# Performance work log

Hardware: AMD Instinct MI355X
Metric: run time of the kernel (lower is better)

The kernel has to match this reference:

```python
import jax, jax.numpy as jnp
import numpy as np

B, S, D, H = 2, 2048, 1024, 16


def setup_inputs() -> dict:
    key = jax.random.key(0)
    kq, kk, kv1, kv2 = jax.random.split(key, 4)
    return {
        "q": jax.random.normal(kq, (B, S, D), dtype=jnp.float32),
        "k": jax.random.normal(kk, (B, S, D), dtype=jnp.float32),
        "v1": jax.random.normal(kv1, (B, S, D), dtype=jnp.float32),
        "v2": jax.random.normal(kv2, (B, S, D), dtype=jnp.float32),
        "num_attn_heads": 16,
    }


def _split_heads(x, h):
    b, s, d = x.shape
    return x.reshape(b, s, h, d // h).transpose(0, 2, 1, 3)  # [B,H,S,dh]


def reference(q, k, v1, v2, num_attn_heads):
    h = num_attn_heads
    b, s, d = q.shape
    dh = d // h
    qh = _split_heads(q, h)
    kh = _split_heads(k, h)
    v1h = _split_heads(v1, h)
    v2h = _split_heads(v2, h)
    scores = jnp.einsum("bhqd,bhkd->bhqk", qh, kh) / jnp.sqrt(jnp.float32(dh))
    # Faithful to create_mask(input, 0): nopeek = triu(ones, k=0); mask = (nopeek == 0)
    # -> only STRICTLY lower triangle is visible; diagonal and above get -1e9.
    # Row 0 is fully masked -> softmax uniform (same as torch behavior).
    allowed = jnp.tril(jnp.ones((s, s), dtype=bool), k=-1)  # [S,S] j < i
    scores = jnp.where(allowed[None, None], scores, jnp.float32(-1e9))
    p_attn = jax.nn.softmax(scores, axis=-1)  # dropout p=0.0 -> identity
    o1 = jnp.einsum("bhqk,bhkd->bhqd", p_attn, v1h)
    o2 = jnp.einsum("bhqk,bhkd->bhqd", p_attn, v2h)
    o1 = o1.transpose(0, 2, 1, 3).reshape(b, s, d)
    o2 = o2.transpose(0, 2, 1, 3).reshape(b, s, d)
    return (o1, o2)
```

## Files before the change

kernel.cpp:

```cpp
#include <hip/hip_runtime.h>

#define B_ 2
#define S_ 2048
#define D_ 1024
#define H_ 16
#define DH 64
#define OFF2 (B_ * S_ * D_)
#define ELEMS (B_ * H_ * S_ * DH)

typedef __attribute__((ext_vector_type(8))) __bf16 bf16x8;
typedef __attribute__((ext_vector_type(4))) float f32x4;
typedef __attribute__((ext_vector_type(4))) unsigned int u32x4;
typedef __attribute__((ext_vector_type(2))) unsigned int u32x2;
typedef __attribute__((address_space(3))) unsigned int lds_u32;
typedef __attribute__((address_space(1))) const unsigned int glob_u32;

__device__ __forceinline__ unsigned short f2bf(float f) {
    return __builtin_bit_cast(unsigned short, (__bf16)f);
}
__device__ __forceinline__ unsigned int pk2(float a, float b) {
    return (unsigned int)f2bf(a) | ((unsigned int)f2bf(b) << 16);
}
__device__ __forceinline__ float bf2f(unsigned short h) {
    unsigned int u = ((unsigned int)h) << 16;
    return __builtin_bit_cast(float, u);
}

__global__ void prep_all(const float* __restrict__ q, const float* __restrict__ k,
                         const float* __restrict__ v1, const float* __restrict__ v2,
                         unsigned short* __restrict__ qb, unsigned short* __restrict__ kb,
                         unsigned short* __restrict__ v1t, unsigned short* __restrict__ v2t) {
    int id = blockIdx.x;
    if (id < 4096) {
        int ysel = id & 1;
        int cid = (id >> 1) * 256 + threadIdx.x;
        const float* src = ysel ? k : q;
        unsigned short* dst = ysel ? kb : qb;
        float scale = ysel ? 1.0f : 0.125f * 1.4426950408889634f;
        int d8 = cid & 7;
        int s  = (cid >> 3) & (S_ - 1);
        int h  = (cid >> 14) & (H_ - 1);
        int b  = cid >> 18;
        int off = (b * S_ + s) * D_ + h * DH + d8 * 8;
        float4 f0 = *(const float4*)(src + off);
        float4 f1 = *(const float4*)(src + off + 4);
        u32x4 wv = {pk2(f0.x * scale, f0.y * scale), pk2(f0.z * scale, f0.w * scale),
                    pk2(f1.x * scale, f1.y * scale), pk2(f1.z * scale, f1.w * scale)};
        *(u32x4*)(dst + cid * 8) = wv;
        return;
    }
    __shared__ __align__(16) unsigned short ldsT[64][72];
    int id2 = id - 4096;
    int t = threadIdx.x;
    int s0 = (id2 & 31) * 64;
    int bh = (id2 >> 5) & 31;
    int b = bh >> 4, h = bh & 15;
    const float* src = (id2 >> 10) ? v2 : v1;
    unsigned short* dst = (id2 >> 10) ? v2t : v1t;
    {
        int sl = t >> 2, dc = t & 3;
        int off = (b * S_ + s0 + sl) * D_ + h * DH + dc * 16;
#pragma unroll
        for (int i4 = 0; i4 < 4; i4++) {
            float4 f = *(const float4*)(src + off + i4 * 4);
            int d = dc * 16 + i4 * 4;
            ldsT[d + 0][sl] = f2bf(f.x);
            ldsT[d + 1][sl] = f2bf(f.y);
            ldsT[d + 2][sl] = f2bf(f.z);
            ldsT[d + 3][sl] = f2bf(f.w);
        }
    }
    __syncthreads();
    {
        int d = t >> 2, sc = t & 3;
        u32x4 a = *(const u32x4*)(&ldsT[d][sc * 16]);
        u32x4 c = *(const u32x4*)(&ldsT[d][sc * 16 + 8]);
        int off = (bh * DH + d) * S_ + s0 + sc * 16;
        *(u32x4*)(dst + off) = a;
        *(u32x4*)(dst + off + 8) = c;
    }
}

__global__ __launch_bounds__(256) void flash_attn(
        const unsigned short* __restrict__ qb, const unsigned short* __restrict__ kb,
        const unsigned short* __restrict__ v1t, const unsigned short* __restrict__ v2t,
        float* __restrict__ out) {
    __shared__ __align__(16) unsigned short sK0[4096], sK1[4096];
    __shared__ __align__(16) unsigned short sV1[4096], sV2[4096];

    int tid = threadIdx.x;
    int w = tid >> 6, lane = tid & 63;
    int lr = lane & 15, lg = lane >> 4;
    int srow = tid >> 3, sco = tid & 7;

    int id = blockIdx.x;
    int xcd = id & 7;
    int j = id >> 3;
    int bh = xcd * 4 + (j & 3);
    int qt = 31 - (j >> 2);
    int b = bh >> 4, hh = bh & 15;

    const unsigned short* gK  = kb  + bh * (S_ * DH);
    const unsigned short* gV1 = v1t + bh * (DH * S_);
    const unsigned short* gV2 = v2t + bh * (DH * S_);

    auto stageV = [&](int t) {
#pragma unroll
        for (int jj = 0; jj < 2; jj++) {
            int row = srow + jj * 32;
            int cosw = (sco ^ (row & 7)) * 8;
            int c8 = (tid + jj * 256) * 8;
            __builtin_amdgcn_global_load_lds((glob_u32*)(gV1 + row * S_ + t * 64 + cosw),
                                             (lds_u32*)(sV1 + c8), 16, 0, 0);
            __builtin_amdgcn_global_load_lds((glob_u32*)(gV2 + row * S_ + t * 64 + cosw),
                                             (lds_u32*)(sV2 + c8), 16, 0, 0);
        }
    };
    auto stageK = [&](unsigned short* dK, int t) {
#pragma unroll
        for (int jj = 0; jj < 2; jj++) {
            int row = srow + jj * 32;
            int cosw = (sco ^ (row & 7)) * 8;
            int c8 = (tid + jj * 256) * 8;
            __builtin_amdgcn_global_load_lds((glob_u32*)(gK + (t * 64 + row) * 64 + cosw),
                                             (lds_u32*)(dK + c8), 16, 0, 0);
        }
    };

    bf16x8 qa[2];
    {
        int qoff = (bh * S_ + qt * 64 + w * 16 + lr) * DH + lg * 8;
        qa[0] = __builtin_bit_cast(bf16x8, *(const u32x4*)(qb + qoff));
        qa[1] = __builtin_bit_cast(bf16x8, *(const u32x4*)(qb + qoff + 32));
    }

    f32x4 acc1[4], acc2[4];
#pragma unroll
    for (int dt = 0; dt < 4; dt++) {
        acc1[dt] = (f32x4){0.f, 0.f, 0.f, 0.f};
        acc2[dt] = (f32x4){0.f, 0.f, 0.f, 0.f};
    }
    float l = 0.f;

    stageK(sK0, 0);

    for (int t = 0; t <= qt; t++) {
        const unsigned short* cK = (t & 1) ? sK1 : sK0;
        unsigned short* nK       = (t & 1) ? sK0 : sK1;
        __builtin_amdgcn_s_barrier();
        stageV(t);
        stageK(nK, (t < qt) ? t + 1 : qt);
        asm volatile("s_waitcnt vmcnt(6)" ::: "memory");
        f32x4 s[4];
        __builtin_amdgcn_s_setprio(1);
#pragma unroll
        for (int n = 0; n < 4; n++) {
            int kv = n * 16 + lr;
            int ix0 = ((kv << 6) + lg * 8) ^ ((kv & 7) << 3);
            int ix1 = ((kv << 6) + 32 + lg * 8) ^ ((kv & 7) << 3);
            bf16x8 k0 = __builtin_bit_cast(bf16x8, *(const u32x4*)(cK + ix0));
            bf16x8 k1 = __builtin_bit_cast(bf16x8, *(const u32x4*)(cK + ix1));
            f32x4 a = __builtin_amdgcn_mfma_f32_16x16x32_bf16(
                k0, qa[0], (f32x4){-20.f, -20.f, -20.f, -20.f}, 0, 0, 0);
            s[n] = __builtin_amdgcn_mfma_f32_16x16x32_bf16(k1, qa[1], a, 0, 0, 0);
        }
        __builtin_amdgcn_s_setprio(0);
        if (t == qt) {
#pragma unroll
            for (int n = 0; n < 4; n++)
#pragma unroll
                for (int r = 0; r < 4; r++)
                    if (n * 16 + lg * 4 + r >= w * 16 + lr) s[n][r] = -1e30f;
        }
        u32x4 pa[2];
#pragma unroll
        for (int ks = 0; ks < 2; ks++) {
            float p0[4], p1[4];
#pragma unroll
            for (int r = 0; r < 4; r++) {
                p0[r] = __builtin_amdgcn_exp2f(s[2 * ks][r]);
                p1[r] = __builtin_amdgcn_exp2f(s[2 * ks + 1][r]);
                l += p0[r] + p1[r];
            }
            unsigned int u0 = pk2(p0[0], p0[1]);
            unsigned int u1 = pk2(p0[2], p0[3]);
            unsigned int u2 = pk2(p1[0], p1[1]);
            unsigned int u3 = pk2(p1[2], p1[3]);
            u32x2 ab = __builtin_amdgcn_permlane32_swap(u0, u2, false, false);
            u32x2 cd = __builtin_amdgcn_permlane32_swap(u1, u3, false, false);
            u32x2 ab2 = __builtin_amdgcn_permlane16_swap(ab[0], ab[1], false, false);
            u32x2 cd2 = __builtin_amdgcn_permlane16_swap(cd[0], cd[1], false, false);
            pa[ks] = (u32x4){ab2[0], cd2[0], ab2[1], cd2[1]};
        }
        asm volatile("s_waitcnt vmcnt(2)" ::: "memory");
        __builtin_amdgcn_s_barrier();
        __builtin_amdgcn_s_setprio(1);
#pragma unroll
        for (int ks = 0; ks < 2; ks++) {
            bf16x8 pab = __builtin_bit_cast(bf16x8, pa[ks]);
#pragma unroll
            for (int dt = 0; dt < 4; dt++) {
                int d = dt * 16 + lr;
                int vix = ((d << 6) + ks * 32 + lg * 8) ^ ((d & 7) << 3);
                bf16x8 vf1 = __builtin_bit_cast(bf16x8, *(const u32x4*)(sV1 + vix));
                acc1[dt] = __builtin_amdgcn_mfma_f32_16x16x32_bf16(vf1, pab, acc1[dt], 0, 0, 0);
                bf16x8 vf2 = __builtin_bit_cast(bf16x8, *(const u32x4*)(sV2 + vix));
                acc2[dt] = __builtin_amdgcn_mfma_f32_16x16x32_bf16(vf2, pab, acc2[dt], 0, 0, 0);
            }
        }
        __builtin_amdgcn_s_setprio(0);
    }

    asm volatile("s_waitcnt vmcnt(0)" ::: "memory");

    float lt = l;
    lt += __shfl_xor(lt, 16, 64);
    lt += __shfl_xor(lt, 32, 64);
    float inv = 1.0f / lt;
    {
        int qrow = qt * 64 + w * 16 + lr;
        int base = (b * S_ + qrow) * D_ + hh * DH + lg * 4;
#pragma unroll
        for (int dt = 0; dt < 4; dt++) {
            f32x4 o1 = acc1[dt] * inv;
            f32x4 o2 = acc2[dt] * inv;
            *(f32x4*)(out + base + dt * 16) = o1;
            *(f32x4*)(out + base + dt * 16 + OFF2) = o2;
        }
    }
}

__global__ void row0_mean(const unsigned short* __restrict__ v1t,
                          const unsigned short* __restrict__ v2t,
                          float* __restrict__ out) {
    int wid = blockIdx.x * 4 + (threadIdx.x >> 6);
    int lane = threadIdx.x & 63;
    int tz = wid >> 11;
    int bhd = wid & 2047;
    const unsigned short* src = (tz ? v2t : v1t) + bhd * S_;
    float sum = 0.f;
#pragma unroll
    for (int kk = 0; kk < 4; kk++) {
        u32x4 v = *(const u32x4*)(src + (kk * 64 + lane) * 8);
#pragma unroll
        for (int jj = 0; jj < 4; jj++) {
            unsigned int u = v[jj];
            sum += bf2f((unsigned short)(u & 0xffff)) + bf2f((unsigned short)(u >> 16));
        }
    }
#pragma unroll
    for (int msk = 32; msk >= 1; msk >>= 1) sum += __shfl_xor(sum, msk, 64);
    if (lane == 0) {
        int b = bhd >> 10, rem = bhd & 1023, h = rem >> 6, d = rem & 63;
        out[tz * OFF2 + b * (S_ * D_) + h * DH + d] = sum * (1.0f / S_);
    }
}

extern "C" void kernel_launch(void* const* d_in, const int* in_sizes, int n_in,
                              void* d_out, int out_size, void* d_ws, size_t ws_size,
                              hipStream_t stream) {
    const float* q  = (const float*)d_in[0];
    const float* k  = (const float*)d_in[1];
    const float* v1 = (const float*)d_in[2];
    const float* v2 = (const float*)d_in[3];
    float* out = (float*)d_out;

    unsigned short* qb  = (unsigned short*)d_ws;
    unsigned short* kb  = qb + ELEMS;
    unsigned short* v1t = kb + ELEMS;
    unsigned short* v2t = v1t + ELEMS;

    prep_all<<<6144, 256, 0, stream>>>(q, k, v1, v2, qb, kb, v1t, v2t);
    flash_attn<<<1024, 256, 0, stream>>>(qb, kb, v1t, v2t, out);
    row0_mean<<<1024, 256, 0, stream>>>(v1t, v2t, out);
}
```

Measured before the change: 70.70 us.

## Fuse Q conversion into attention kernel and compute row sums via MFMA

Q is no longer converted to bf16 in the prep kernel. The attention kernel now reads fp32 Q directly, then scales and packs it in registers. This removes a full write and read of the Q workspace and shrinks the prep grid. The softmax denominator is now accumulated with an extra MFMA against a ones vector instead of scalar adds and cross-lane shuffles. The last tile is peeled, so the redundant K prefetch on the final iteration is dropped.

Result: faster. 66.88 us (-5.4%).

```diff
diff --git a/kernel.cpp b/kernel.cpp
--- a/kernel.cpp
+++ b/kernel.cpp
@@ -26,31 +26,27 @@
     return __builtin_bit_cast(float, u);
 }
 
-__global__ void prep_all(const float* __restrict__ q, const float* __restrict__ k,
+__global__ void prep_all(const float* __restrict__ k,
                          const float* __restrict__ v1, const float* __restrict__ v2,
-                         unsigned short* __restrict__ qb, unsigned short* __restrict__ kb,
+                         unsigned short* __restrict__ kb,
                          unsigned short* __restrict__ v1t, unsigned short* __restrict__ v2t) {
     int id = blockIdx.x;
-    if (id < 4096) {
-        int ysel = id & 1;
-        int cid = (id >> 1) * 256 + threadIdx.x;
-        const float* src = ysel ? k : q;
-        unsigned short* dst = ysel ? kb : qb;
-        float scale = ysel ? 1.0f : 0.125f * 1.4426950408889634f;
+    if (id < 2048) {
+        int cid = id * 256 + threadIdx.x;
         int d8 = cid & 7;
         int s  = (cid >> 3) & (S_ - 1);
         int h  = (cid >> 14) & (H_ - 1);
         int b  = cid >> 18;
         int off = (b * S_ + s) * D_ + h * DH + d8 * 8;
-        float4 f0 = *(const float4*)(src + off);
-        float4 f1 = *(const float4*)(src + off + 4);
-        u32x4 wv = {pk2(f0.x * scale, f0.y * scale), pk2(f0.z * scale, f0.w * scale),
-                    pk2(f1.x * scale, f1.y * scale), pk2(f1.z * scale, f1.w * scale)};
-        *(u32x4*)(dst + cid * 8) = wv;
+        float4 f0 = *(const float4*)(k + off);
+        float4 f1 = *(const float4*)(k + off + 4);
+        u32x4 wv = {pk2(f0.x, f0.y), pk2(f0.z, f0.w),
+                    pk2(f1.x, f1.y), pk2(f1.z, f1.w)};
+        *(u32x4*)(kb + cid * 8) = wv;
         return;
     }
     __shared__ __align__(16) unsigned short ldsT[64][72];
-    int id2 = id - 4096;
+    int id2 = id - 2048;
     int t = threadIdx.x;
     int s0 = (id2 & 31) * 64;
     int bh = (id2 >> 5) & 31;
@@ -82,7 +78,7 @@
 }
 
 __global__ __launch_bounds__(256) void flash_attn(
-        const unsigned short* __restrict__ qb, const unsigned short* __restrict__ kb,
+        const float* __restrict__ qf, const unsigned short* __restrict__ kb,
         const unsigned short* __restrict__ v1t, const unsigned short* __restrict__ v2t,
         float* __restrict__ out) {
     __shared__ __align__(16) unsigned short sK0[4096], sK1[4096];
@@ -129,28 +125,32 @@
 
     bf16x8 qa[2];
     {
-        int qoff = (bh * S_ + qt * 64 + w * 16 + lr) * DH + lg * 8;
-        qa[0] = __builtin_bit_cast(bf16x8, *(const u32x4*)(qb + qoff));
-        qa[1] = __builtin_bit_cast(bf16x8, *(const u32x4*)(qb + qoff + 32));
-    }
-
-    f32x4 acc1[4], acc2[4];
+        const float qs = 0.125f * 1.4426950408889634f;
+        const float* a = qf + ((size_t)b * S_ + qt * 64 + w * 16 + lr) * D_ + hh * DH + lg * 8;
+        float4 q0 = *(const float4*)a;
+        float4 q1 = *(const float4*)(a + 4);
+        float4 q2 = *(const float4*)(a + 32);
+        float4 q3 = *(const float4*)(a + 36);
+        u32x4 w0 = {pk2(q0.x * qs, q0.y * qs), pk2(q0.z * qs, q0.w * qs),
+                    pk2(q1.x * qs, q1.y * qs), pk2(q1.z * qs, q1.w * qs)};
+        u32x4 w1 = {pk2(q2.x * qs, q2.y * qs), pk2(q2.z * qs, q2.w * qs),
+                    pk2(q3.x * qs, q3.y * qs), pk2(q3.z * qs, q3.w * qs)};
+        qa[0] = __builtin_bit_cast(bf16x8, w0);
+        qa[1] = __builtin_bit_cast(bf16x8, w1);
+    }
+
+    const u32x4 onesu = {0x3F803F80u, 0x3F803F80u, 0x3F803F80u, 0x3F803F80u};
+    const bf16x8 ones = __builtin_bit_cast(bf16x8, onesu);
+
+    f32x4 acc1[4], acc2[4], lacc;
 #pragma unroll
     for (int dt = 0; dt < 4; dt++) {
         acc1[dt] = (f32x4){0.f, 0.f, 0.f, 0.f};
         acc2[dt] = (f32x4){0.f, 0.f, 0.f, 0.f};
     }
-    float l = 0.f;
-
-    stageK(sK0, 0);
-
-    for (int t = 0; t <= qt; t++) {
-        const unsigned short* cK = (t & 1) ? sK1 : sK0;
-        unsigned short* nK       = (t & 1) ? sK0 : sK1;
-        __builtin_amdgcn_s_barrier();
-        stageV(t);
-        stageK(nK, (t < qt) ? t + 1 : qt);
-        asm volatile("s_waitcnt vmcnt(6)" ::: "memory");
+    lacc = (f32x4){0.f, 0.f, 0.f, 0.f};
+
+    auto iterBody = [&](int t, const unsigned short* cK, bool last) {
         f32x4 s[4];
         __builtin_amdgcn_s_setprio(1);
 #pragma unroll
@@ -165,7 +165,7 @@
             s[n] = __builtin_amdgcn_mfma_f32_16x16x32_bf16(k1, qa[1], a, 0, 0, 0);
         }
         __builtin_amdgcn_s_setprio(0);
-        if (t == qt) {
+        if (last) {
 #pragma unroll
             for (int n = 0; n < 4; n++)
 #pragma unroll
@@ -180,7 +180,6 @@
             for (int r = 0; r < 4; r++) {
                 p0[r] = __builtin_amdgcn_exp2f(s[2 * ks][r]);
                 p1[r] = __builtin_amdgcn_exp2f(s[2 * ks + 1][r]);
-                l += p0[r] + p1[r];
             }
             unsigned int u0 = pk2(p0[0], p0[1]);
             unsigned int u1 = pk2(p0[2], p0[3]);
@@ -192,12 +191,14 @@
             u32x2 cd2 = __builtin_amdgcn_permlane16_swap(cd[0], cd[1], false, false);
             pa[ks] = (u32x4){ab2[0], cd2[0], ab2[1], cd2[1]};
         }
-        asm volatile("s_waitcnt vmcnt(2)" ::: "memory");
+        if (last) asm volatile("s_waitcnt vmcnt(0)" ::: "memory");
+        else      asm volatile("s_waitcnt vmcnt(2)" ::: "memory");
         __builtin_amdgcn_s_barrier();
         __builtin_amdgcn_s_setprio(1);
 #pragma unroll
         for (int ks = 0; ks < 2; ks++) {
             bf16x8 pab = __builtin_bit_cast(bf16x8, pa[ks]);
+            lacc = __builtin_amdgcn_mfma_f32_16x16x32_bf16(ones, pab, lacc, 0, 0, 0);
 #pragma unroll
             for (int dt = 0; dt < 4; dt++) {
                 int d = dt * 16 + lr;
@@ -209,14 +210,28 @@
             }
         }
         __builtin_amdgcn_s_setprio(0);
-    }
-
-    asm volatile("s_waitcnt vmcnt(0)" ::: "memory");
-
-    float lt = l;
-    lt += __shfl_xor(lt, 16, 64);
-    lt += __shfl_xor(lt, 32, 64);
-    float inv = 1.0f / lt;
+    };
+
+    stageK(sK0, 0);
+    int t = 0;
+    for (; t < qt; t++) {
+        const unsigned short* cK = (t & 1) ? sK1 : sK0;
+        unsigned short* nK       = (t & 1) ? sK0 : sK1;
+        __builtin_amdgcn_s_barrier();
+        stageV(t);
+        stageK(nK, t + 1);
+        asm volatile("s_waitcnt vmcnt(6)" ::: "memory");
+        iterBody(t, cK, false);
+    }
+    {
+        const unsigned short* cK = (t & 1) ? sK1 : sK0;
+        __builtin_amdgcn_s_barrier();
+        stageV(t);
+        asm volatile("s_waitcnt vmcnt(4)" ::: "memory");
+        iterBody(t, cK, true);
+    }
+
+    float inv = 1.0f / lacc[0];
     {
         int qrow = qt * 64 + w * 16 + lr;
         int base = (b * S_ + qrow) * D_ + hh * DH + lg * 4;
@@ -265,12 +280,11 @@
     const float* v2 = (const float*)d_in[3];
     float* out = (float*)d_out;
 
-    unsigned short* qb  = (unsigned short*)d_ws;
-    unsigned short* kb  = qb + ELEMS;
+    unsigned short* kb  = (unsigned short*)d_ws;
     unsigned short* v1t = kb + ELEMS;
     unsigned short* v2t = v1t + ELEMS;
 
-    prep_all<<<6144, 256, 0, stream>>>(q, k, v1, v2, qb, kb, v1t, v2t);
-    flash_attn<<<1024, 256, 0, stream>>>(qb, kb, v1t, v2t, out);
+    prep_all<<<4096, 256, 0, stream>>>(k, v1, v2, kb, v1t, v2t);
+    flash_attn<<<1024, 256, 0, stream>>>(q, kb, v1t, v2t, out);
     row0_mean<<<1024, 256, 0, stream>>>(v1t, v2t, out);
 }
```

## Split V1/V2 across wave pairs, exchanging P tiles through LDS

Applied to the files above, without the earlier changes.

Each wave now reads only one of the two V tiles (waves 0-1 use V1, waves 2-3 use V2). Each wave writes its bf16 P fragment to LDS so its partner wave can multiply it against the same V, which halves V LDS reads per wave. Row sums are now computed by an MFMA against a vector of ones, using the bf16-rounded P, instead of scalar adds. The cost is an extra LDS tile, an LDS write/read and wait per iteration, and two extra MFMAs per k-step.

New measurement: 72.68 us. +2.8%, slower.

```diff
diff --git a/kernel.cpp b/kernel.cpp
--- a/kernel.cpp
+++ b/kernel.cpp
@@ -87,6 +87,7 @@
         float* __restrict__ out) {
     __shared__ __align__(16) unsigned short sK0[4096], sK1[4096];
     __shared__ __align__(16) unsigned short sV1[4096], sV2[4096];
+    __shared__ __align__(16) unsigned short sPT[4096];
 
     int tid = threadIdx.x;
     int w = tid >> 6, lane = tid & 63;
@@ -134,13 +135,20 @@
         qa[1] = __builtin_bit_cast(bf16x8, *(const u32x4*)(qb + qoff + 32));
     }
 
-    f32x4 acc1[4], acc2[4];
+    int tz = w >> 1, pw = w ^ 2;
+    const unsigned short* cV = tz ? sV2 : sV1;
+
+    const u32x4 onesu = {0x3F803F80u, 0x3F803F80u, 0x3F803F80u, 0x3F803F80u};
+    const bf16x8 ones = __builtin_bit_cast(bf16x8, onesu);
+
+    f32x4 accO[4], accP[4], laccO, laccP;
 #pragma unroll
     for (int dt = 0; dt < 4; dt++) {
-        acc1[dt] = (f32x4){0.f, 0.f, 0.f, 0.f};
-        acc2[dt] = (f32x4){0.f, 0.f, 0.f, 0.f};
-    }
-    float l = 0.f;
+        accO[dt] = (f32x4){0.f, 0.f, 0.f, 0.f};
+        accP[dt] = (f32x4){0.f, 0.f, 0.f, 0.f};
+    }
+    laccO = (f32x4){0.f, 0.f, 0.f, 0.f};
+    laccP = (f32x4){0.f, 0.f, 0.f, 0.f};
 
     stageK(sK0, 0);
 
@@ -169,18 +177,17 @@
 #pragma unroll
             for (int n = 0; n < 4; n++)
 #pragma unroll
-                for (int r = 0; r < 4; r++)
-                    if (n * 16 + lg * 4 + r >= w * 16 + lr) s[n][r] = -1e30f;
+                for (int rr = 0; rr < 4; rr++)
+                    if (n * 16 + lg * 4 + rr >= w * 16 + lr) s[n][rr] = -1e30f;
         }
         u32x4 pa[2];
 #pragma unroll
         for (int ks = 0; ks < 2; ks++) {
             float p0[4], p1[4];
 #pragma unroll
-            for (int r = 0; r < 4; r++) {
-                p0[r] = __builtin_amdgcn_exp2f(s[2 * ks][r]);
-                p1[r] = __builtin_amdgcn_exp2f(s[2 * ks + 1][r]);
-                l += p0[r] + p1[r];
+            for (int rr = 0; rr < 4; rr++) {
+                p0[rr] = __builtin_amdgcn_exp2f(s[2 * ks][rr]);
+                p1[rr] = __builtin_amdgcn_exp2f(s[2 * ks + 1][rr]);
             }
             unsigned int u0 = pk2(p0[0], p0[1]);
             unsigned int u1 = pk2(p0[2], p0[3]);
@@ -192,20 +199,27 @@
             u32x2 cd2 = __builtin_amdgcn_permlane16_swap(cd[0], cd[1], false, false);
             pa[ks] = (u32x4){ab2[0], cd2[0], ab2[1], cd2[1]};
         }
+        *(u32x4*)(sPT + w * 1024 + lane * 8) = pa[0];
+        *(u32x4*)(sPT + w * 1024 + 512 + lane * 8) = pa[1];
+        asm volatile("s_waitcnt lgkmcnt(0)" ::: "memory");
         asm volatile("s_waitcnt vmcnt(2)" ::: "memory");
         __builtin_amdgcn_s_barrier();
+        u32x4 paP0 = *(const u32x4*)(sPT + pw * 1024 + lane * 8);
+        u32x4 paP1 = *(const u32x4*)(sPT + pw * 1024 + 512 + lane * 8);
         __builtin_amdgcn_s_setprio(1);
 #pragma unroll
         for (int ks = 0; ks < 2; ks++) {
-            bf16x8 pab = __builtin_bit_cast(bf16x8, pa[ks]);
+            bf16x8 pab  = __builtin_bit_cast(bf16x8, pa[ks]);
+            bf16x8 pabP = __builtin_bit_cast(bf16x8, ks ? paP1 : paP0);
+            laccO = __builtin_amdgcn_mfma_f32_16x16x32_bf16(ones, pab,  laccO, 0, 0, 0);
+            laccP = __builtin_amdgcn_mfma_f32_16x16x32_bf16(ones, pabP, laccP, 0, 0, 0);
 #pragma unroll
             for (int dt = 0; dt < 4; dt++) {
                 int d = dt * 16 + lr;
                 int vix = ((d << 6) + ks * 32 + lg * 8) ^ ((d & 7) << 3);
-                bf16x8 vf1 = __builtin_bit_cast(bf16x8, *(const u32x4*)(sV1 + vix));
-                acc1[dt] = __builtin_amdgcn_mfma_f32_16x16x32_bf16(vf1, pab, acc1[dt], 0, 0, 0);
-                bf16x8 vf2 = __builtin_bit_cast(bf16x8, *(const u32x4*)(sV2 + vix));
-                acc2[dt] = __builtin_amdgcn_mfma_f32_16x16x32_bf16(vf2, pab, acc2[dt], 0, 0, 0);
+                bf16x8 vf = __builtin_bit_cast(bf16x8, *(const u32x4*)(cV + vix));
+                accO[dt] = __builtin_amdgcn_mfma_f32_16x16x32_bf16(vf, pab,  accO[dt], 0, 0, 0);
+                accP[dt] = __builtin_amdgcn_mfma_f32_16x16x32_bf16(vf, pabP, accP[dt], 0, 0, 0);
             }
         }
         __builtin_amdgcn_s_setprio(0);
@@ -213,19 +227,19 @@
 
     asm volatile("s_waitcnt vmcnt(0)" ::: "memory");
 
-    float lt = l;
-    lt += __shfl_xor(lt, 16, 64);
-    lt += __shfl_xor(lt, 32, 64);
-    float inv = 1.0f / lt;
-    {
-        int qrow = qt * 64 + w * 16 + lr;
-        int base = (b * S_ + qrow) * D_ + hh * DH + lg * 4;
+    {
+        float invO = 1.0f / laccO[0];
+        float invP = 1.0f / laccP[0];
+        int qO = qt * 64 + w * 16 + lr;
+        int qP = qt * 64 + pw * 16 + lr;
+        int baseO = (b * S_ + qO) * D_ + hh * DH + lg * 4 + tz * OFF2;
+        int baseP = (b * S_ + qP) * D_ + hh * DH + lg * 4 + tz * OFF2;
 #pragma unroll
         for (int dt = 0; dt < 4; dt++) {
-            f32x4 o1 = acc1[dt] * inv;
-            f32x4 o2 = acc2[dt] * inv;
-            *(f32x4*)(out + base + dt * 16) = o1;
-            *(f32x4*)(out + base + dt * 16 + OFF2) = o2;
+            f32x4 oO = accO[dt] * invO;
+            f32x4 oP = accP[dt] * invP;
+            *(f32x4*)(out + baseO + dt * 16) = oO;
+            *(f32x4*)(out + baseP + dt * 16) = oP;
         }
     }
 }
```
